# Kernel optimization log

Hardware: AMD Instinct MI355X
Metric: run time of the kernel (lower is better)

Reference implementation:

```python
import jax, jax.numpy as jnp
import numpy as np

D_MODEL = 256
N_HEADS = 8
N_LEVELS = 4
N_POINTS = 4
HEAD_DIM = D_MODEL // N_HEADS
SPATIAL = [(64, 64), (32, 32), (16, 16), (8, 8)]
LEN_IN = sum(h * w for h, w in SPATIAL)
BATCH = 4
LEN_Q = LEN_IN


def _offset_bias():
    # replicate the module's _reset_parameters grid init for sampling_offsets.bias
    th = np.arange(N_HEADS, dtype=np.float64) * (2.0 * np.pi / N_HEADS)
    g = np.stack([np.cos(th), np.sin(th)], -1)
    g = g / np.abs(g).max(-1, keepdims=True)
    g = np.tile(g[:, None, None, :], (1, N_LEVELS, N_POINTS, 1))
    g = g * (np.arange(N_POINTS) + 1)[None, None, :, None]
    return jnp.asarray(g.reshape(-1), jnp.float32)


def setup_inputs() -> dict:
    key = jax.random.key(0)
    ks = jax.random.split(key, 10)
    s = 1.0 / np.sqrt(D_MODEL)
    return {
        "query": jax.random.normal(ks[0], (BATCH, LEN_Q, D_MODEL), jnp.float32),
        "reference_points": jax.random.uniform(ks[1], (BATCH, LEN_Q, N_LEVELS, 2), jnp.float32),
        "input_flatten": jax.random.normal(ks[2], (BATCH, LEN_IN, D_MODEL), jnp.float32),
        "input_spatial_shapes": np.array(SPATIAL, dtype=np.int64),
        "input_level_start_index": np.cumsum([0] + [h * w for h, w in SPATIAL[:-1]]).astype(np.int64),
        "W_val": jax.random.normal(ks[3], (D_MODEL, D_MODEL), jnp.float32) * s,
        "b_val": jnp.zeros((D_MODEL,), jnp.float32),
        "W_off": jax.random.normal(ks[4], (D_MODEL, N_HEADS * N_LEVELS * N_POINTS * 2), jnp.float32) * 0.01,
        "b_off": _offset_bias(),
        "W_attn": jax.random.normal(ks[5], (D_MODEL, N_HEADS * N_LEVELS * N_POINTS), jnp.float32) * 0.01,
        "b_attn": jnp.zeros((N_HEADS * N_LEVELS * N_POINTS,), jnp.float32),
        "W_out": jax.random.normal(ks[6], (D_MODEL, D_MODEL), jnp.float32) * s,
        "b_out": jnp.zeros((D_MODEL,), jnp.float32),
    }


def bilinear_sample(v, grid):
    # v: [B, C, H, W]; grid: [B, Q, P, 2] normalized to [-1, 1] (x=W axis, y=H axis)
    # matches torch F.grid_sample(mode='bilinear', padding_mode='zeros', align_corners=False)
    B, C, H, W = v.shape
    x = (grid[..., 0] + 1.0) * (W * 0.5) - 0.5
    y = (grid[..., 1] + 1.0) * (H * 0.5) - 0.5
    x0 = jnp.floor(x)
    y0 = jnp.floor(y)
    wx = x - x0
    wy = y - y0
    v_flat = v.reshape(B, C, H * W)

    def corner(xi, yi, wgt):
        valid = (xi >= 0) & (xi <= W - 1) & (yi >= 0) & (yi <= H - 1)
        xc = jnp.clip(xi, 0, W - 1).astype(jnp.int32)
        yc = jnp.clip(yi, 0, H - 1).astype(jnp.int32)
        idx = (yc * W + xc).reshape(B, 1, -1)
        g = jnp.take_along_axis(v_flat, jnp.broadcast_to(idx, (B, C, idx.shape[-1])), axis=2)
        return g * (wgt * valid).reshape(B, 1, -1)

    out = (corner(x0, y0, (1 - wx) * (1 - wy))
           + corner(x0 + 1, y0, wx * (1 - wy))
           + corner(x0, y0 + 1, (1 - wx) * wy)
           + corner(x0 + 1, y0 + 1, wx * wy))
    return out.reshape(B, C, grid.shape[1], grid.shape[2])


def reference(query, reference_points, input_flatten, input_spatial_shapes,
              input_level_start_index, W_val, b_val, W_off, b_off,
              W_attn, b_attn, W_out, b_out):
    ss = np.asarray(input_spatial_shapes)  # static [L, 2] (H, W)
    Nb, Lq, _ = query.shape
    value = (input_flatten @ W_val + b_val).reshape(Nb, -1, N_HEADS, HEAD_DIM)
    off = (query @ W_off + b_off).reshape(Nb, Lq, N_HEADS, N_LEVELS, N_POINTS, 2)
    attn = (query @ W_attn + b_attn).reshape(Nb, Lq, N_HEADS, N_LEVELS * N_POINTS)
    attn = jax.nn.softmax(attn, -1).reshape(Nb, Lq, N_HEADS, N_LEVELS, N_POINTS)
    # offset normalizer: (W, H) per level
    normalizer = jnp.asarray(ss[:, ::-1].copy(), jnp.float32)
    loc = reference_points[:, :, None, :, None, :] + off / normalizer[None, None, None, :, None, :]
    grids = 2.0 * loc - 1.0  # [N, Lq, H, L, P, 2]
    splits = np.cumsum([int(h) * int(w) for h, w in ss])[:-1]
    value_list = jnp.split(value, splits, axis=1)
    out = jnp.zeros((Nb * N_HEADS, HEAD_DIM, Lq), query.dtype)
    for lid, (h, w) in enumerate(ss):
        h, w = int(h), int(w)
        v = value_list[lid].transpose(0, 2, 3, 1).reshape(Nb * N_HEADS, HEAD_DIM, h, w)
        g = grids[:, :, :, lid].transpose(0, 2, 1, 3, 4).reshape(Nb * N_HEADS, Lq, N_POINTS, 2)
        sampled = bilinear_sample(v, g)  # [N*H, D, Lq, P]
        aw = attn[:, :, :, lid].transpose(0, 2, 1, 3).reshape(Nb * N_HEADS, 1, Lq, N_POINTS)
        out = out + (sampled * aw).sum(-1)
    out = out.reshape(Nb, N_HEADS * HEAD_DIM, Lq).transpose(0, 2, 1)
    return out @ W_out + b_out
```

## Files before the change

kernel.cpp:

```cpp
#include <hip/hip_runtime.h>
#include <hip/hip_bf16.h>
#include <math.h>

typedef unsigned short ushort_t;
typedef __attribute__((ext_vector_type(8))) short bf16x8;
typedef __attribute__((ext_vector_type(4))) float f32x4;
typedef __attribute__((ext_vector_type(2))) float f32x2;

constexpr int BATCH   = 4;
constexpr int D_MODEL = 256;
constexpr int LEN_IN  = 5440;
constexpr int LEN_Q   = 5440;
constexpr int M_TOT   = BATCH * LEN_Q;

#define ASG __attribute__((address_space(1)))
#define ASL __attribute__((address_space(3)))

__device__ __forceinline__ void gld16(const void* g, void* l) {
    __builtin_amdgcn_global_load_lds((ASG const void*)g, (ASL void*)l, 16, 0, 0);
}

__device__ __forceinline__ ushort_t bfbits(float x) {
    __hip_bfloat16 h = __float2bfloat16(x);
    ushort_t u; __builtin_memcpy(&u, &h, 2); return u;
}
__device__ __forceinline__ unsigned pk2(float a, float b) {
    return (unsigned)bfbits(a) | ((unsigned)bfbits(b) << 16);
}

__global__ __launch_bounds__(256) void pack_inputs(
    const float* __restrict__ inflat, const float* __restrict__ query,
    const float* __restrict__ Wv, const float* __restrict__ Wo,
    const float* __restrict__ Wa, const float* __restrict__ Wout,
    const float* __restrict__ b_off, const float* __restrict__ b_attn,
    ushort_t* __restrict__ in_bf, ushort_t* __restrict__ q_bf,
    ushort_t* __restrict__ wvT, ushort_t* __restrict__ woaT,
    ushort_t* __restrict__ woutT, float* __restrict__ bias_oa)
{
    const int blk = blockIdx.x, tid = threadIdx.x;
    if (blk < 5440) {
        const float* src = (blk < 2720) ? inflat : query;
        ushort_t*    dst = (blk < 2720) ? in_bf : q_bf;
        const int rb = (blk < 2720) ? blk : blk - 2720;
        const size_t base = (size_t)rb * 2048 + tid * 8;
        float4 a = *(const float4*)(src + base);
        float4 b = *(const float4*)(src + base + 4);
        uint4 o;
        o.x = pk2(a.x, a.y); o.y = pk2(a.z, a.w);
        o.z = pk2(b.x, b.y); o.w = pk2(b.z, b.w);
        *(uint4*)(dst + base) = o;
    } else if (blk < 5504) {
        const float* src = (blk < 5472) ? Wv : Wout;
        ushort_t*    dst = (blk < 5472) ? wvT : woutT;
        const int base = (blk - ((blk < 5472) ? 5440 : 5472)) * 2048;
#pragma unroll
        for (int i = 0; i < 8; i++) {
            const int idx = base + i * 256 + tid;
            const int k = idx >> 8, n = idx & 255;
            dst[n * 256 + k] = bfbits(src[idx]);
        }
    } else if (blk < 5552) {
        const int base = (blk - 5504) * 2048;
#pragma unroll
        for (int i = 0; i < 8; i++) {
            const int idx = base + i * 256 + tid;
            const int k = idx / 384, j = idx - k * 384;
            const float v = (j < 256) ? Wo[k * 256 + j] : Wa[k * 128 + (j - 256)];
            woaT[j * 256 + k] = bfbits(v);
        }
    } else {
        bias_oa[tid] = b_off[tid];
        if (tid < 128) bias_oa[256 + tid] = b_attn[tid];
    }
}

template <int OUT_MODE>
__device__ __forceinline__ void gemm_core(
    const ushort_t* __restrict__ A, const ushort_t* __restrict__ BT,
    const float* __restrict__ bias, void* __restrict__ Cp, int N,
    int bm, int bn, ushort_t* As, ushort_t* Bs)
{
    const int tid  = threadIdx.x;
    const int wave = tid >> 6, lane = tid & 63;
    const int wm = (wave >> 1) * 64, wn = (wave & 1) * 64;
    const int c0 = 2 * wave, c1 = 2 * wave + 1;
    const int kb = (lane & 3) * 8;
    const ushort_t* gA0 = A  + (size_t)(bm + c0 * 16 + (lane >> 2)) * 256 + kb;
    const ushort_t* gA1 = A  + (size_t)(bm + c1 * 16 + (lane >> 2)) * 256 + kb;
    const ushort_t* gB0 = BT + (size_t)(bn + c0 * 16 + (lane >> 2)) * 256 + kb;
    const ushort_t* gB1 = BT + (size_t)(bn + c1 * 16 + (lane >> 2)) * 256 + kb;
    ushort_t* lA0 = As + c0 * 512;
    ushort_t* lA1 = As + c1 * 512;
    ushort_t* lB0 = Bs + c0 * 512;
    ushort_t* lB1 = Bs + c1 * 512;

    f32x4 acc[4][4] = {};

    const int row = lane & 15, kg = (lane >> 4) * 8;
    for (int kt = 0; kt < 8; kt++) {
        gld16(gA0, lA0); gld16(gA1, lA1);
        gld16(gB0, lB0); gld16(gB1, lB1);
        gA0 += 32; gA1 += 32; gB0 += 32; gB1 += 32;
        __syncthreads();
        bf16x8 af[4], bfr[4];
#pragma unroll
        for (int i = 0; i < 4; i++)
            af[i] = *(const bf16x8*)(As + (wm + i * 16 + row) * 32 + kg);
#pragma unroll
        for (int j = 0; j < 4; j++)
            bfr[j] = *(const bf16x8*)(Bs + (wn + j * 16 + row) * 32 + kg);
#pragma unroll
        for (int i = 0; i < 4; i++)
#pragma unroll
            for (int j = 0; j < 4; j++)
                acc[i][j] = __builtin_amdgcn_mfma_f32_16x16x32_bf16(
                    af[i], bfr[j], acc[i][j], 0, 0, 0);
        __syncthreads();
    }

    const int col = lane & 15, rbase = (lane >> 4) * 4;
#pragma unroll
    for (int j = 0; j < 4; j++) {
        const int cc = bn + wn + j * 16 + col;
        const float bv = bias[cc];
#pragma unroll
        for (int i = 0; i < 4; i++) {
            const int rr = bm + wm + i * 16 + rbase;
#pragma unroll
            for (int r = 0; r < 4; r++) {
                const float v = acc[i][j][r] + bv;
                const int m = rr + r;
                if (OUT_MODE == 0) {
                    ((float*)Cp)[(size_t)m * N + cc] = v;
                } else if (OUT_MODE == 1) {
                    ((ushort_t*)Cp)[(size_t)m * N + cc] = bfbits(v);
                } else {
                    const int bb  = m / LEN_IN;
                    const int pix = m - bb * LEN_IN;
                    const int head = cc >> 5, ch = cc & 31;
                    ((ushort_t*)Cp)[((size_t)((bb * 8 + head) * LEN_IN + pix) << 5) + ch] = bfbits(v);
                }
            }
        }
    }
}

__global__ __launch_bounds__(256) void gemm_dual(
    const ushort_t* __restrict__ in_bf, const ushort_t* __restrict__ wvT,
    const float* __restrict__ b_val, ushort_t* __restrict__ value_bf,
    const ushort_t* __restrict__ q_bf, const ushort_t* __restrict__ woaT,
    const float* __restrict__ bias_oa, float* __restrict__ offattn)
{
    __shared__ ushort_t As[128 * 32];
    __shared__ ushort_t Bs[128 * 32];
    int blk = blockIdx.x;
    if (blk < 340) {
        const int bn = (blk & 1) * 128, bm = (blk >> 1) * 128;
        gemm_core<2>(in_bf, wvT, b_val, value_bf, 256, bm, bn, As, Bs);
    } else {
        blk -= 340;
        const int bn = (blk % 3) * 128, bm = (blk / 3) * 128;
        gemm_core<0>(q_bf, woaT, bias_oa, offattn, 384, bm, bn, As, Bs);
    }
}

__global__ __launch_bounds__(256) void gemm_out(
    const ushort_t* __restrict__ mid_bf, const ushort_t* __restrict__ woutT,
    const float* __restrict__ b_out, float* __restrict__ out)
{
    __shared__ ushort_t As[128 * 32];
    __shared__ ushort_t Bs[128 * 32];
    const int bn = (blockIdx.x & 1) * 128, bm = (blockIdx.x >> 1) * 128;
    gemm_core<0>(mid_bf, woutT, b_out, out, 256, bm, bn, As, Bs);
}

__device__ __forceinline__ void accd(f32x2& a, unsigned u, f32x2 w) {
    f32x2 v;
    v.x = __uint_as_float(u << 16);
    v.y = __uint_as_float(u & 0xFFFF0000u);
    a = w * v + a;
}
__device__ __forceinline__ void accp(f32x2* a, uint4 u, float wf) {
    const f32x2 w = {wf, wf};
    accd(a[0], u.x, w); accd(a[1], u.y, w);
    accd(a[2], u.z, w); accd(a[3], u.w, w);
}

__global__ __launch_bounds__(256) void msda_sample_v3(
    const ushort_t* __restrict__ value,
    const float* __restrict__ refp,
    const float* __restrict__ offattn,
    ushort_t* __restrict__ mid)
{
    const int tid = threadIdx.x;
    const unsigned bid = blockIdx.x;
    const int xcd   = bid & 7;
    const int pos   = bid >> 3;
    const int slice = pos / 85;
    const int qc    = pos - slice * 85;
    const int bh    = xcd * 4 + slice;
    const int b     = bh >> 3, h = bh & 7;

    const int ql = tid >> 2;
    const int cg = tid & 3;
    const int bq = b * LEN_Q + qc * 64 + ql;

    const float* oab = offattn + (size_t)bq * 384;
    const float* lp = oab + 256 + h * 16;
    float4 l0 = ((const float4*)lp)[0];
    float4 l1 = ((const float4*)lp)[1];
    float4 l2 = ((const float4*)lp)[2];
    float4 l3 = ((const float4*)lp)[3];
    float lg[16] = {l0.x, l0.y, l0.z, l0.w, l1.x, l1.y, l1.z, l1.w,
                    l2.x, l2.y, l2.z, l2.w, l3.x, l3.y, l3.z, l3.w};
    float mx = lg[0];
#pragma unroll
    for (int j = 1; j < 16; j++) mx = fmaxf(mx, lg[j]);

    const float* op = oab + h * 32;
    float4 ov[8];
#pragma unroll
    for (int j = 0; j < 8; j++) ov[j] = ((const float4*)op)[j];
    const float* rp = refp + (size_t)bq * 8;
    float4 r0 = ((const float4*)rp)[0];
    float4 r1 = ((const float4*)rp)[1];
    const float rx[4] = {r0.x, r0.z, r1.x, r1.z};
    const float ry[4] = {r0.y, r0.w, r1.y, r1.w};

    const char* vb = (const char*)value + (size_t)bh * (LEN_IN * 64) + cg * 16;

    f32x2 acc2[4];
#pragma unroll
    for (int d = 0; d < 4; d++) acc2[d] = (f32x2){0.f, 0.f};
    float esum = 0.f;

#pragma unroll
    for (int l = 0; l < 4; l++) {
        const int   shift = 6 - l;
        const int   W     = 1 << shift;
        const float fW    = (float)W;
        const float invW  = __uint_as_float((unsigned)(127 - shift) << 23);
        const int   st    = (l == 0) ? 0 : (l == 1) ? 4096 : (l == 2) ? 5120 : 5376;
#pragma unroll
        for (int p = 0; p < 4; p++) {
            const float* o2 = &ov[l * 2].x;
            const float ox = o2[p * 2 + 0];
            const float oy = o2[p * 2 + 1];
            const float x = (rx[l] + ox * invW) * fW - 0.5f;
            const float y = (ry[l] + oy * invW) * fW - 0.5f;
            const float x0f = floorf(x), y0f = floorf(y);
            const float wx = x - x0f, wy = y - y0f;
            const int ix0 = (int)x0f, iy0 = (int)y0f;
            const int ix1 = ix0 + 1,  iy1 = iy0 + 1;
            const float vx0 = (ix0 >= 0 && ix0 < W) ? 1.f : 0.f;
            const float vx1 = (ix1 >= 0 && ix1 < W) ? 1.f : 0.f;
            const float vy0 = (iy0 >= 0 && iy0 < W) ? 1.f : 0.f;
            const float vy1 = (iy1 >= 0 && iy1 < W) ? 1.f : 0.f;
            const int cx0 = min(max(ix0, 0), W - 1);
            const int cx1 = min(max(ix1, 0), W - 1);
            const int cy0 = min(max(iy0, 0), W - 1);
            const int cy1 = min(max(iy1, 0), W - 1);
            const float hx0 = (1.f - wx) * vx0, hx1 = wx * vx1;
            const float hy0 = (1.f - wy) * vy0, hy1 = wy * vy1;

            const float e = __expf(lg[l * 4 + p] - mx);
            esum += e;
            const float w00 = e * hx0 * hy0, w01 = e * hx1 * hy0;
            const float w10 = e * hx0 * hy1, w11 = e * hx1 * hy1;

            const int r0a = st + (cy0 << shift);
            const int r1a = st + (cy1 << shift);
            uint4 v00 = *(const uint4*)(vb + ((size_t)(r0a + cx0) << 6));
            uint4 v01 = *(const uint4*)(vb + ((size_t)(r0a + cx1) << 6));
            uint4 v10 = *(const uint4*)(vb + ((size_t)(r1a + cx0) << 6));
            uint4 v11 = *(const uint4*)(vb + ((size_t)(r1a + cx1) << 6));

            accp(acc2, v00, w00);
            accp(acc2, v01, w01);
            accp(acc2, v10, w10);
            accp(acc2, v11, w11);
        }
    }

    const float inv = 1.f / esum;
    uint4 o;
    o.x = pk2(acc2[0].x * inv, acc2[0].y * inv);
    o.y = pk2(acc2[1].x * inv, acc2[1].y * inv);
    o.z = pk2(acc2[2].x * inv, acc2[2].y * inv);
    o.w = pk2(acc2[3].x * inv, acc2[3].y * inv);
    ((uint4*)(mid + (size_t)bq * 256 + h * 32))[cg] = o;
}

extern "C" void kernel_launch(void* const* d_in, const int* in_sizes, int n_in,
                              void* d_out, int out_size, void* d_ws, size_t ws_size,
                              hipStream_t stream)
{
    const float* query  = (const float*)d_in[0];
    const float* refp   = (const float*)d_in[1];
    const float* inflat = (const float*)d_in[2];
    const float* W_val  = (const float*)d_in[5];
    const float* b_val  = (const float*)d_in[6];
    const float* W_off  = (const float*)d_in[7];
    const float* W_attn = (const float*)d_in[9];
    const float* b_off  = (const float*)d_in[8];
    const float* b_attn = (const float*)d_in[10];
    const float* W_out  = (const float*)d_in[11];
    const float* b_out  = (const float*)d_in[12];
    float* out = (float*)d_out;

    char* ws = (char*)d_ws;
    ushort_t* in_bf    = (ushort_t*)ws;
    ushort_t* q_bf     = (ushort_t*)(ws + 11141120);
    ushort_t* value_bf = (ushort_t*)(ws + 22282240);
    ushort_t* wvT      = (ushort_t*)(ws + 33423360);
    ushort_t* woutT    = (ushort_t*)(ws + 33554432);
    ushort_t* woaT     = (ushort_t*)(ws + 33685504);
    float*    bias_oa  = (float*)   (ws + 33882112);
    float*    offattn  = (float*)   (ws + 33883648);
    ushort_t* mid_bf   = in_bf;

    dim3 blk(256);
    pack_inputs<<<dim3(5553), blk, 0, stream>>>(
        inflat, query, W_val, W_off, W_attn, W_out, b_off, b_attn,
        in_bf, q_bf, wvT, woaT, woutT, bias_oa);
    gemm_dual<<<dim3(850), blk, 0, stream>>>(
        in_bf, wvT, b_val, value_bf, q_bf, woaT, bias_oa, offattn);
    msda_sample_v3<<<dim3(2720), blk, 0, stream>>>(
        value_bf, refp, offattn, mid_bf);
    gemm_out<<<dim3(340), blk, 0, stream>>>(
        mid_bf, woutT, b_out, out);
}
```

Measured before the change: 195.9 us.

## Fuse fp32-to-bf16 activation conversion into GEMM A-tile loads

The separate pack pass that converted input_flatten and query to bf16 is removed. The dual GEMM now reads fp32 activations directly and converts them to bf16 while writing the A tile to LDS, which removes a full read-write round trip of two 22 MB tensors. The weight pack kernel now reads coalesced and writes 16-byte transposed stores, and the sampler loads offsets and reference points per level instead of all at once. The cost is that the GEMM A loads become synchronous register loads in place of async global-to-LDS loads, and fp32 traffic per GEMM tile doubles.

Result: faster. 184.0 us (-6.1%).

```diff
diff --git a/kernel.cpp b/kernel.cpp
--- a/kernel.cpp
+++ b/kernel.cpp
@@ -28,55 +28,48 @@
     return (unsigned)bfbits(a) | ((unsigned)bfbits(b) << 16);
 }
 
-__global__ __launch_bounds__(256) void pack_inputs(
-    const float* __restrict__ inflat, const float* __restrict__ query,
-    const float* __restrict__ Wv, const float* __restrict__ Wo,
-    const float* __restrict__ Wa, const float* __restrict__ Wout,
+__global__ __launch_bounds__(256) void pack_weights(
+    const float* __restrict__ Wv, const float* __restrict__ Wout,
+    const float* __restrict__ Wo, const float* __restrict__ Wa,
     const float* __restrict__ b_off, const float* __restrict__ b_attn,
-    ushort_t* __restrict__ in_bf, ushort_t* __restrict__ q_bf,
-    ushort_t* __restrict__ wvT, ushort_t* __restrict__ woaT,
-    ushort_t* __restrict__ woutT, float* __restrict__ bias_oa)
-{
-    const int blk = blockIdx.x, tid = threadIdx.x;
-    if (blk < 5440) {
-        const float* src = (blk < 2720) ? inflat : query;
-        ushort_t*    dst = (blk < 2720) ? in_bf : q_bf;
-        const int rb = (blk < 2720) ? blk : blk - 2720;
-        const size_t base = (size_t)rb * 2048 + tid * 8;
-        float4 a = *(const float4*)(src + base);
-        float4 b = *(const float4*)(src + base + 4);
-        uint4 o;
-        o.x = pk2(a.x, a.y); o.y = pk2(a.z, a.w);
-        o.z = pk2(b.x, b.y); o.w = pk2(b.z, b.w);
-        *(uint4*)(dst + base) = o;
-    } else if (blk < 5504) {
-        const float* src = (blk < 5472) ? Wv : Wout;
-        ushort_t*    dst = (blk < 5472) ? wvT : woutT;
-        const int base = (blk - ((blk < 5472) ? 5440 : 5472)) * 2048;
-#pragma unroll
-        for (int i = 0; i < 8; i++) {
-            const int idx = base + i * 256 + tid;
-            const int k = idx >> 8, n = idx & 255;
-            dst[n * 256 + k] = bfbits(src[idx]);
-        }
-    } else if (blk < 5552) {
-        const int base = (blk - 5504) * 2048;
-#pragma unroll
-        for (int i = 0; i < 8; i++) {
-            const int idx = base + i * 256 + tid;
-            const int k = idx / 384, j = idx - k * 384;
-            const float v = (j < 256) ? Wo[k * 256 + j] : Wa[k * 128 + (j - 256)];
-            woaT[j * 256 + k] = bfbits(v);
+    ushort_t* __restrict__ wvT, ushort_t* __restrict__ woutT,
+    ushort_t* __restrict__ woaT, float* __restrict__ bias_oa)
+{
+    const int blk = blockIdx.x, t = threadIdx.x;
+    if (blk < 64) {
+        const float* src = (blk < 32) ? Wv : Wout;
+        ushort_t*    dst = (blk < 32) ? wvT : woutT;
+        const int k0 = (blk & 31) * 8;
+        float f[8];
+#pragma unroll
+        for (int i = 0; i < 8; i++) f[i] = src[(k0 + i) * 256 + t];
+        *(uint4*)(dst + t * 256 + k0) =
+            make_uint4(pk2(f[0], f[1]), pk2(f[2], f[3]),
+                       pk2(f[4], f[5]), pk2(f[6], f[7]));
+    } else if (blk < 96) {
+        const int k0 = (blk - 64) * 8;
+#pragma unroll
+        for (int rep = 0; rep < 2; rep++) {
+            const int j = (rep == 0) ? t : 256 + t;
+            if (rep == 1 && t >= 128) break;
+            float f[8];
+#pragma unroll
+            for (int i = 0; i < 8; i++)
+                f[i] = (j < 256) ? Wo[(k0 + i) * 256 + j]
+                                 : Wa[(k0 + i) * 128 + (j - 256)];
+            *(uint4*)(woaT + j * 256 + k0) =
+                make_uint4(pk2(f[0], f[1]), pk2(f[2], f[3]),
+                           pk2(f[4], f[5]), pk2(f[6], f[7]));
         }
     } else {
-        bias_oa[tid] = b_off[tid];
-        if (tid < 128) bias_oa[256 + tid] = b_attn[tid];
-    }
-}
-
-template <int OUT_MODE>
+        bias_oa[t] = b_off[t];
+        if (t < 128) bias_oa[256 + t] = b_attn[t];
+    }
+}
+
+template <int OUT_MODE, bool A_F32>
 __device__ __forceinline__ void gemm_core(
-    const ushort_t* __restrict__ A, const ushort_t* __restrict__ BT,
+    const void* __restrict__ Ap, const ushort_t* __restrict__ BT,
     const float* __restrict__ bias, void* __restrict__ Cp, int N,
     int bm, int bn, ushort_t* As, ushort_t* Bs)
 {
@@ -85,8 +78,17 @@
     const int wm = (wave >> 1) * 64, wn = (wave & 1) * 64;
     const int c0 = 2 * wave, c1 = 2 * wave + 1;
     const int kb = (lane & 3) * 8;
-    const ushort_t* gA0 = A  + (size_t)(bm + c0 * 16 + (lane >> 2)) * 256 + kb;
-    const ushort_t* gA1 = A  + (size_t)(bm + c1 * 16 + (lane >> 2)) * 256 + kb;
+    const int ar0 = bm + c0 * 16 + (lane >> 2);
+    const int ar1 = bm + c1 * 16 + (lane >> 2);
+    const ushort_t* gA0h = nullptr; const ushort_t* gA1h = nullptr;
+    const float*    gA0f = nullptr; const float*    gA1f = nullptr;
+    if (A_F32) {
+        gA0f = (const float*)Ap + (size_t)ar0 * 256 + kb;
+        gA1f = (const float*)Ap + (size_t)ar1 * 256 + kb;
+    } else {
+        gA0h = (const ushort_t*)Ap + (size_t)ar0 * 256 + kb;
+        gA1h = (const ushort_t*)Ap + (size_t)ar1 * 256 + kb;
+    }
     const ushort_t* gB0 = BT + (size_t)(bn + c0 * 16 + (lane >> 2)) * 256 + kb;
     const ushort_t* gB1 = BT + (size_t)(bn + c1 * 16 + (lane >> 2)) * 256 + kb;
     ushort_t* lA0 = As + c0 * 512;
@@ -95,12 +97,26 @@
     ushort_t* lB1 = Bs + c1 * 512;
 
     f32x4 acc[4][4] = {};
-
     const int row = lane & 15, kg = (lane >> 4) * 8;
     for (int kt = 0; kt < 8; kt++) {
-        gld16(gA0, lA0); gld16(gA1, lA1);
+        if (A_F32) {
+            float4 a0 = *(const float4*)gA0f;
+            float4 a1 = *(const float4*)(gA0f + 4);
+            float4 b0 = *(const float4*)gA1f;
+            float4 b1 = *(const float4*)(gA1f + 4);
+            *(uint4*)(lA0 + lane * 8) =
+                make_uint4(pk2(a0.x, a0.y), pk2(a0.z, a0.w),
+                           pk2(a1.x, a1.y), pk2(a1.z, a1.w));
+            *(uint4*)(lA1 + lane * 8) =
+                make_uint4(pk2(b0.x, b0.y), pk2(b0.z, b0.w),
+                           pk2(b1.x, b1.y), pk2(b1.z, b1.w));
+            gA0f += 32; gA1f += 32;
+        } else {
+            gld16(gA0h, lA0); gld16(gA1h, lA1);
+            gA0h += 32; gA1h += 32;
+        }
         gld16(gB0, lB0); gld16(gB1, lB1);
-        gA0 += 32; gA1 += 32; gB0 += 32; gB1 += 32;
+        gB0 += 32; gB1 += 32;
         __syncthreads();
         bf16x8 af[4], bfr[4];
 #pragma unroll
@@ -132,8 +148,6 @@
                 const int m = rr + r;
                 if (OUT_MODE == 0) {
                     ((float*)Cp)[(size_t)m * N + cc] = v;
-                } else if (OUT_MODE == 1) {
-                    ((ushort_t*)Cp)[(size_t)m * N + cc] = bfbits(v);
                 } else {
                     const int bb  = m / LEN_IN;
                     const int pix = m - bb * LEN_IN;
@@ -146,9 +160,9 @@
 }
 
 __global__ __launch_bounds__(256) void gemm_dual(
-    const ushort_t* __restrict__ in_bf, const ushort_t* __restrict__ wvT,
+    const float* __restrict__ inflat, const ushort_t* __restrict__ wvT,
     const float* __restrict__ b_val, ushort_t* __restrict__ value_bf,
-    const ushort_t* __restrict__ q_bf, const ushort_t* __restrict__ woaT,
+    const float* __restrict__ query, const ushort_t* __restrict__ woaT,
     const float* __restrict__ bias_oa, float* __restrict__ offattn)
 {
     __shared__ ushort_t As[128 * 32];
@@ -156,11 +170,11 @@
     int blk = blockIdx.x;
     if (blk < 340) {
         const int bn = (blk & 1) * 128, bm = (blk >> 1) * 128;
-        gemm_core<2>(in_bf, wvT, b_val, value_bf, 256, bm, bn, As, Bs);
+        gemm_core<2, true>(inflat, wvT, b_val, value_bf, 256, bm, bn, As, Bs);
     } else {
         blk -= 340;
         const int bn = (blk % 3) * 128, bm = (blk / 3) * 128;
-        gemm_core<0>(q_bf, woaT, bias_oa, offattn, 384, bm, bn, As, Bs);
+        gemm_core<0, true>(query, woaT, bias_oa, offattn, 384, bm, bn, As, Bs);
     }
 }
 
@@ -171,7 +185,7 @@
     __shared__ ushort_t As[128 * 32];
     __shared__ ushort_t Bs[128 * 32];
     const int bn = (blockIdx.x & 1) * 128, bm = (blockIdx.x >> 1) * 128;
-    gemm_core<0>(mid_bf, woutT, b_out, out, 256, bm, bn, As, Bs);
+    gemm_core<0, false>(mid_bf, woutT, b_out, out, 256, bm, bn, As, Bs);
 }
 
 __device__ __forceinline__ void accd(f32x2& a, unsigned u, f32x2 w) {
@@ -218,14 +232,7 @@
     for (int j = 1; j < 16; j++) mx = fmaxf(mx, lg[j]);
 
     const float* op = oab + h * 32;
-    float4 ov[8];
-#pragma unroll
-    for (int j = 0; j < 8; j++) ov[j] = ((const float4*)op)[j];
     const float* rp = refp + (size_t)bq * 8;
-    float4 r0 = ((const float4*)rp)[0];
-    float4 r1 = ((const float4*)rp)[1];
-    const float rx[4] = {r0.x, r0.z, r1.x, r1.z};
-    const float ry[4] = {r0.y, r0.w, r1.y, r1.w};
 
     const char* vb = (const char*)value + (size_t)bh * (LEN_IN * 64) + cg * 16;
 
@@ -241,13 +248,16 @@
         const float fW    = (float)W;
         const float invW  = __uint_as_float((unsigned)(127 - shift) << 23);
         const int   st    = (l == 0) ? 0 : (l == 1) ? 4096 : (l == 2) ? 5120 : 5376;
+
+        const float2 rl = *(const float2*)(rp + l * 2);
+        const float4 oA = ((const float4*)op)[l * 2];
+        const float4 oB = ((const float4*)op)[l * 2 + 1];
+        const float oxA[4] = {oA.x, oA.z, oB.x, oB.z};
+        const float oyA[4] = {oA.y, oA.w, oB.y, oB.w};
 #pragma unroll
         for (int p = 0; p < 4; p++) {
-            const float* o2 = &ov[l * 2].x;
-            const float ox = o2[p * 2 + 0];
-            const float oy = o2[p * 2 + 1];
-            const float x = (rx[l] + ox * invW) * fW - 0.5f;
-            const float y = (ry[l] + oy * invW) * fW - 0.5f;
+            const float x = (rl.x + oxA[p] * invW) * fW - 0.5f;
+            const float y = (rl.y + oyA[p] * invW) * fW - 0.5f;
             const float x0f = floorf(x), y0f = floorf(y);
             const float wx = x - x0f, wy = y - y0f;
             const int ix0 = (int)x0f, iy0 = (int)y0f;
@@ -309,22 +319,20 @@
     float* out = (float*)d_out;
 
     char* ws = (char*)d_ws;
-    ushort_t* in_bf    = (ushort_t*)ws;
-    ushort_t* q_bf     = (ushort_t*)(ws + 11141120);
-    ushort_t* value_bf = (ushort_t*)(ws + 22282240);
-    ushort_t* wvT      = (ushort_t*)(ws + 33423360);
-    ushort_t* woutT    = (ushort_t*)(ws + 33554432);
-    ushort_t* woaT     = (ushort_t*)(ws + 33685504);
-    float*    bias_oa  = (float*)   (ws + 33882112);
-    float*    offattn  = (float*)   (ws + 33883648);
-    ushort_t* mid_bf   = in_bf;
+    ushort_t* mid_bf   = (ushort_t*)ws;
+    ushort_t* value_bf = (ushort_t*)(ws + 11141120);
+    ushort_t* wvT      = (ushort_t*)(ws + 22282240);
+    ushort_t* woutT    = (ushort_t*)(ws + 22413312);
+    ushort_t* woaT     = (ushort_t*)(ws + 22544384);
+    float*    bias_oa  = (float*)   (ws + 22740992);
+    float*    offattn  = (float*)   (ws + 22742528);
 
     dim3 blk(256);
-    pack_inputs<<<dim3(5553), blk, 0, stream>>>(
-        inflat, query, W_val, W_off, W_attn, W_out, b_off, b_attn,
-        in_bf, q_bf, wvT, woaT, woutT, bias_oa);
+    pack_weights<<<dim3(97), blk, 0, stream>>>(
+        W_val, W_out, W_off, W_attn, b_off, b_attn,
+        wvT, woutT, woaT, bias_oa);
     gemm_dual<<<dim3(850), blk, 0, stream>>>(
-        in_bf, wvT, b_val, value_bf, q_bf, woaT, bias_oa, offattn);
+        inflat, wvT, b_val, value_bf, query, woaT, bias_oa, offattn);
     msda_sample_v3<<<dim3(2720), blk, 0, stream>>>(
         value_bf, refp, offattn, mid_bf);
     gemm_out<<<dim3(340), blk, 0, stream>>>(
```
